# Kernel tuning notes

Hardware: AMD Instinct MI355X
Metric: run time of the kernel (lower is better)

The kernel has to match this reference:

```python
import jax, jax.numpy as jnp
import numpy as np

B, N, H, V = 8192, 12, 512, 256  # batch, n_columns, hidden_size, per-column vocab
LN_EPS = 1e-5


def setup_inputs() -> dict:
    key = jax.random.key(0)
    k0, k1, k2, k3 = jax.random.split(key, 4)
    return {
        "input_embedding": jax.random.normal(k0, (B, H), dtype=jnp.float32),
        "features": jax.random.randint(k1, (B, N), 0, V),  # one categorical id per column
        "emb_tables": jax.random.normal(k2, (N, V, H), dtype=jnp.float32) * 0.02,
        "ln_gamma": jnp.ones((2 * H,), dtype=jnp.float32),
        "ln_beta": jnp.zeros((2 * H,), dtype=jnp.float32),
        "pred_W": jax.random.normal(k3, (N, 2 * H, V), dtype=jnp.float32) * 0.02,
        "pred_b": jnp.zeros((N, V), dtype=jnp.float32),
    }


def reference(input_embedding, features, emb_tables, ln_gamma, ln_beta, pred_W, pred_b):
    n = features.shape[1]
    # per-column embedding lookup: emb[b, n] = emb_tables[n, features[b, n]]  -> [B, N, H]
    emb = emb_tables[jnp.arange(n)[None, :], features]
    # _make_masked_sums: triu(diagonal=1) mask summed over dim 1 == exclusive prefix sum
    # over the column axis: masked_sums[b, j] = sum_{i < j} emb[b, i]
    masked_sums = jnp.cumsum(emb, axis=1) - emb  # [B, N, H]
    ctx = jnp.broadcast_to(input_embedding[:, None, :], emb.shape)  # [B, N, H]
    x = jnp.concatenate([ctx, masked_sums], axis=-1)  # [B, N, 2H]
    # LayerNorm over last dim, then exact (erf) GELU as in torch nn.GELU default
    mu = jnp.mean(x, axis=-1, keepdims=True)
    var = jnp.mean(jnp.square(x - mu), axis=-1, keepdims=True)
    xn = (x - mu) * jax.lax.rsqrt(var + LN_EPS) * ln_gamma + ln_beta
    act = jax.nn.gelu(xn, approximate=False)
    # per-column predictor heads: logits[b, n, :] = act[b, n, :] @ pred_W[n] + pred_b[n]
    logits = jnp.einsum('bnh,nhv->bnv', act, pred_W) + pred_b
    return logits
```

## Files before the change

### kernel.cpp

```cpp
#include <hip/hip_runtime.h>
#include <stdint.h>

#define B_SZ 8192
#define N_F 12
#define H_DIM 512
#define K_DIM 1024
#define V_DIM 256

typedef __attribute__((ext_vector_type(8))) __bf16 bf16x8;
typedef __attribute__((ext_vector_type(4))) float f32x4;

__device__ inline float gelu_f(float x) {
  float t = 1.5957691216057308f * x * (1.0f + 0.044715f * x * x);
  return x / (1.0f + __expf(-t));
}

__device__ inline void gld_lds16(const void* g, void* l) {
  __builtin_amdgcn_global_load_lds(
      (const __attribute__((address_space(1))) void*)g,
      (__attribute__((address_space(3))) void*)l, 16, 0, 0);
}

__global__ __launch_bounds__(256, 8) void k_prep(
    const float* __restrict__ ie, const int* __restrict__ feat,
    const float* __restrict__ tab, const float* __restrict__ gam,
    const float* __restrict__ bet, __bf16* __restrict__ act2,
    float* __restrict__ stats) {
  const int lane = threadIdx.x & 63;
  const int b = blockIdx.x * 4 + (threadIdx.x >> 6);

  const float* cb = ie + (size_t)b * H_DIM + lane * 8;
  float4 c0 = *(const float4*)cb;
  float4 c1 = *(const float4*)(cb + 4);
  float s = c0.x + c0.y + c0.z + c0.w + c1.x + c1.y + c1.z + c1.w;
  float q = c0.x * c0.x + c0.y * c0.y + c0.z * c0.z + c0.w * c0.w +
            c1.x * c1.x + c1.y * c1.y + c1.z * c1.z + c1.w * c1.w;
#pragma unroll
  for (int o = 1; o < 64; o <<= 1) {
    s += __shfl_xor(s, o, 64);
    q += __shfl_xor(q, o, 64);
  }
  const float S1 = s, Q1 = q;

  const float4 g0 = *(const float4*)(gam + H_DIM + lane * 8);
  const float4 g1 = *(const float4*)(gam + H_DIM + lane * 8 + 4);
  const float4 e0 = *(const float4*)(bet + H_DIM + lane * 8);
  const float4 e1 = *(const float4*)(bet + H_DIM + lane * 8 + 4);

  float r[8];
#pragma unroll
  for (int i = 0; i < 8; ++i) r[i] = 0.f;

  const int sw = (lane & ~7) | ((lane & 7) ^ (b & 7));
  __bf16* arow = act2 + (size_t)b * H_DIM + sw * 8;

  for (int n = 0; n < N_F; ++n) {
    s = 0.f; q = 0.f;
#pragma unroll
    for (int i = 0; i < 8; ++i) { s += r[i]; q += r[i] * r[i]; }
#pragma unroll
    for (int o = 1; o < 64; o <<= 1) {
      s += __shfl_xor(s, o, 64);
      q += __shfl_xor(q, o, 64);
    }
    const float mean = (S1 + s) * (1.0f / 1024.0f);
    const float var = (Q1 + q) * (1.0f / 1024.0f) - mean * mean;
    const float rs = rsqrtf(var + 1e-5f);
    if (lane == 0)
      *(float2*)(stats + ((size_t)b * N_F + n) * 2) = make_float2(mean, rs);

    float4 t0, t1;
    const bool have = (n < N_F - 1);
    if (have) {
      const int f = feat[b * N_F + n];
      const float* tr = tab + ((size_t)n * V_DIM + f) * H_DIM + lane * 8;
      t0 = *(const float4*)tr;
      t1 = *(const float4*)(tr + 4);
    }

    bf16x8 pk;
    pk[0] = (__bf16)gelu_f((r[0] - mean) * rs * g0.x + e0.x);
    pk[1] = (__bf16)gelu_f((r[1] - mean) * rs * g0.y + e0.y);
    pk[2] = (__bf16)gelu_f((r[2] - mean) * rs * g0.z + e0.z);
    pk[3] = (__bf16)gelu_f((r[3] - mean) * rs * g0.w + e0.w);
    pk[4] = (__bf16)gelu_f((r[4] - mean) * rs * g1.x + e1.x);
    pk[5] = (__bf16)gelu_f((r[5] - mean) * rs * g1.y + e1.y);
    pk[6] = (__bf16)gelu_f((r[6] - mean) * rs * g1.z + e1.z);
    pk[7] = (__bf16)gelu_f((r[7] - mean) * rs * g1.w + e1.w);
    *(bf16x8*)(arow + (size_t)n * B_SZ * H_DIM) = pk;

    if (have) {
      r[0] += t0.x; r[1] += t0.y; r[2] += t0.z; r[3] += t0.w;
      r[4] += t1.x; r[5] += t1.y; r[6] += t1.z; r[7] += t1.w;
    }
  }
}

__global__ __launch_bounds__(256) void k_wt(const float* __restrict__ W,
                                            __bf16* __restrict__ Wt) {
  __shared__ float tile[32][33];
  const int bid = blockIdx.x;
  const int n = bid >> 8;
  const int rem = bid & 255;
  const int kt = rem >> 3, vt = rem & 7;
  const int tx = threadIdx.x & 31, ty = threadIdx.x >> 5;
  const float* src = W + (size_t)n * K_DIM * V_DIM;
#pragma unroll
  for (int i = 0; i < 4; ++i) {
    const int k = kt * 32 + ty + i * 8;
    tile[ty + i * 8][tx] = src[(size_t)k * V_DIM + vt * 32 + tx];
  }
  __syncthreads();
  __bf16* dst = Wt + (size_t)n * V_DIM * K_DIM;
  const int t = threadIdx.x;
  if (t < 128) {
    const int v_l = t >> 2, c_l = t & 3;
    const int v = vt * 32 + v_l;
    bf16x8 pk;
#pragma unroll
    for (int e = 0; e < 8; ++e) pk[e] = (__bf16)tile[c_l * 8 + e][v_l];
    const int gc = kt * 4 + c_l;
    const int swc = (gc & ~7) | ((gc & 7) ^ (v & 7));
    *(bf16x8*)(dst + (size_t)v * K_DIM + swc * 8) = pk;
  }
}

__global__ __launch_bounds__(512, 2) void k_gemm(
    const float* __restrict__ ie, const __bf16* __restrict__ act2,
    const __bf16* __restrict__ Wt, const float* __restrict__ stats,
    const float* __restrict__ gam, const float* __restrict__ bet,
    const float* __restrict__ bias, float* __restrict__ out) {
  constexpr int BM = 128, BN = 256, BK = 64;
  __shared__ __align__(16) __bf16 As[2][BM * BK];
  __shared__ __align__(16) __bf16 Ws[2][BN * BK];

  const int n = blockIdx.y;
  const int b0 = blockIdx.x * BM;
  const int t = threadIdx.x;
  const int lane = t & 63;
  const int w = t >> 6;
  const int wm = w & 1;
  const int wn = w >> 1;
  const int l15 = lane & 15;
  const int lq = lane >> 4;
  const int lr8 = lane >> 3;
  const int lo8 = lane & 7;

  const __bf16* act2n = act2 + (size_t)n * B_SZ * H_DIM;
  const __bf16* Wtn = Wt + (size_t)n * V_DIM * K_DIM;

  {
    const int k0 = 0;
#pragma unroll
    for (int p = 0; p < 4; ++p) {
      const int v0 = w * 32 + p * 8;
      gld_lds16(Wtn + (size_t)(v0 + lr8) * K_DIM + k0 + lo8 * 8,
                &Ws[0][v0 * BK]);
    }
  }

  const int pr = t >> 2;
  const int pm = t & 3;
  bf16x8 ctx[16];
  {
    const float2 st = *(const float2*)(stats + ((size_t)(b0 + pr) * N_F + n) * 2);
    const float mu = st.x, rs = st.y;
    const float* ierow = ie + (size_t)(b0 + pr) * H_DIM;
#pragma unroll
    for (int k8 = 0; k8 < 8; ++k8) {
#pragma unroll
      for (int h = 0; h < 2; ++h) {
        const int col = k8 * 64 + pm * 16 + h * 8;
        const float4 x0 = *(const float4*)(ierow + col);
        const float4 x1 = *(const float4*)(ierow + col + 4);
        const float4 gg0 = *(const float4*)(gam + col);
        const float4 gg1 = *(const float4*)(gam + col + 4);
        const float4 bb0 = *(const float4*)(bet + col);
        const float4 bb1 = *(const float4*)(bet + col + 4);
        bf16x8 pk;
        pk[0] = (__bf16)gelu_f((x0.x - mu) * rs * gg0.x + bb0.x);
        pk[1] = (__bf16)gelu_f((x0.y - mu) * rs * gg0.y + bb0.y);
        pk[2] = (__bf16)gelu_f((x0.z - mu) * rs * gg0.z + bb0.z);
        pk[3] = (__bf16)gelu_f((x0.w - mu) * rs * gg0.w + bb0.w);
        pk[4] = (__bf16)gelu_f((x1.x - mu) * rs * gg1.x + bb1.x);
        pk[5] = (__bf16)gelu_f((x1.y - mu) * rs * gg1.y + bb1.y);
        pk[6] = (__bf16)gelu_f((x1.z - mu) * rs * gg1.z + bb1.z);
        pk[7] = (__bf16)gelu_f((x1.w - mu) * rs * gg1.w + bb1.w);
        ctx[k8 * 2 + h] = pk;
      }
    }
  }

  const int sA0 = pr * BK + (((pm * 2) ^ (pr & 7)) << 3);
  const int sA1 = pr * BK + (((pm * 2 + 1) ^ (pr & 7)) << 3);

  f32x4 acc[4][4];
#pragma unroll
  for (int i = 0; i < 4; ++i)
#pragma unroll
    for (int j = 0; j < 4; ++j) acc[i][j] = (f32x4){0.f, 0.f, 0.f, 0.f};

  *(bf16x8*)(&As[0][sA0]) = ctx[0];
  *(bf16x8*)(&As[0][sA1]) = ctx[1];
  __syncthreads();

  int cur = 0;
#pragma unroll
  for (int kt = 0; kt < 16; ++kt) {
    if (kt < 15) {
      const int k0 = (kt + 1) * BK;
#pragma unroll
      for (int p = 0; p < 4; ++p) {
        const int v0 = w * 32 + p * 8;
        gld_lds16(Wtn + (size_t)(v0 + lr8) * K_DIM + k0 + lo8 * 8,
                  &Ws[cur ^ 1][v0 * BK]);
      }
      if (kt + 1 < 8) {
        *(bf16x8*)(&As[cur ^ 1][sA0]) = ctx[(kt + 1) * 2];
        *(bf16x8*)(&As[cur ^ 1][sA1]) = ctx[(kt + 1) * 2 + 1];
      } else {
#pragma unroll
        for (int p = 0; p < 2; ++p) {
          const int r0 = w * 16 + p * 8;
          gld_lds16(act2n + (size_t)(b0 + r0 + lr8) * H_DIM + (k0 - H_DIM) + lo8 * 8,
                    &As[cur ^ 1][r0 * BK]);
        }
      }
    }
#pragma unroll
    for (int ks = 0; ks < 2; ++ks) {
      const int cs = ks * 4 + lq;
      bf16x8 af[4], bb[4];
#pragma unroll
      for (int i = 0; i < 4; ++i) {
        const int row = wm * 64 + i * 16 + l15;
        af[i] = *(const bf16x8*)(&As[cur][row * BK + ((cs ^ (row & 7)) << 3)]);
      }
#pragma unroll
      for (int j = 0; j < 4; ++j) {
        const int row = wn * 64 + j * 16 + l15;
        bb[j] = *(const bf16x8*)(&Ws[cur][row * BK + ((cs ^ (row & 7)) << 3)]);
      }
#pragma unroll
      for (int i = 0; i < 4; ++i)
#pragma unroll
        for (int j = 0; j < 4; ++j)
          acc[i][j] = __builtin_amdgcn_mfma_f32_16x16x32_bf16(af[i], bb[j],
                                                              acc[i][j], 0, 0, 0);
    }
    __syncthreads();
    cur ^= 1;
  }

#pragma unroll
  for (int j = 0; j < 4; ++j) {
    const int v = wn * 64 + j * 16 + l15;
    const float bv = bias[n * V_DIM + v];
#pragma unroll
    for (int i = 0; i < 4; ++i) {
      const int rb = wm * 64 + i * 16 + lq * 4;
#pragma unroll
      for (int r = 0; r < 4; ++r) {
        out[((size_t)(b0 + rb + r) * N_F + n) * V_DIM + v] = acc[i][j][r] + bv;
      }
    }
  }
}

extern "C" void kernel_launch(void* const* d_in, const int* in_sizes, int n_in,
                              void* d_out, int out_size, void* d_ws, size_t ws_size,
                              hipStream_t stream) {
  const float* ie = (const float*)d_in[0];
  const int* feat = (const int*)d_in[1];
  const float* tab = (const float*)d_in[2];
  const float* gam = (const float*)d_in[3];
  const float* bet = (const float*)d_in[4];
  const float* predW = (const float*)d_in[5];
  const float* predb = (const float*)d_in[6];
  float* out = (float*)d_out;

  char* ws = (char*)d_ws;
  __bf16* act2 = (__bf16*)ws;
  float* stats = (float*)(ws + 100663296);
  __bf16* Wt = (__bf16*)(ws + 100663296 + 786432);

  hipLaunchKernelGGL(k_prep, dim3(B_SZ / 4), dim3(256), 0, stream, ie, feat,
                     tab, gam, bet, act2, stats);
  hipLaunchKernelGGL(k_wt, dim3(3072), dim3(256), 0, stream, predW, Wt);
  hipLaunchKernelGGL(k_gemm, dim3(B_SZ / 128, N_F), dim3(512), 0, stream, ie,
                     act2, Wt, stats, gam, bet, predb, out);
}
```

Before: 275.4 us.

## Store activations in the output buffer in place and single-buffer GEMM LDS

The bf16 activation scratch is moved into the output buffer and laid out as [b][n][h], so each (b,n) slot has the same byte size as its logits row. Each GEMM block reads only the activation rows it later overwrites with logits, which lets the workspace shrink and keeps activation and output traffic on the same addresses. To make the in-place overwrite safe and simplify the loop, the GEMM drops LDS double buffering in favour of single buffers with two barriers per K step. The risk is losing overlap between global-to-LDS loads and MFMA compute.

```diff
diff --git a/kernel.cpp b/kernel.cpp
--- a/kernel.cpp
+++ b/kernel.cpp
@@ -24,7 +24,7 @@
 __global__ __launch_bounds__(256, 8) void k_prep(
     const float* __restrict__ ie, const int* __restrict__ feat,
     const float* __restrict__ tab, const float* __restrict__ gam,
-    const float* __restrict__ bet, __bf16* __restrict__ act2,
+    const float* __restrict__ bet, __bf16* actA,
     float* __restrict__ stats) {
   const int lane = threadIdx.x & 63;
   const int b = blockIdx.x * 4 + (threadIdx.x >> 6);
@@ -52,7 +52,7 @@
   for (int i = 0; i < 8; ++i) r[i] = 0.f;
 
   const int sw = (lane & ~7) | ((lane & 7) ^ (b & 7));
-  __bf16* arow = act2 + (size_t)b * H_DIM + sw * 8;
+  __bf16* arow = actA + (size_t)b * N_F * H_DIM + sw * 8;
 
   for (int n = 0; n < N_F; ++n) {
     s = 0.f; q = 0.f;
@@ -87,7 +87,7 @@
     pk[5] = (__bf16)gelu_f((r[5] - mean) * rs * g1.y + e1.y);
     pk[6] = (__bf16)gelu_f((r[6] - mean) * rs * g1.z + e1.z);
     pk[7] = (__bf16)gelu_f((r[7] - mean) * rs * g1.w + e1.w);
-    *(bf16x8*)(arow + (size_t)n * B_SZ * H_DIM) = pk;
+    *(bf16x8*)(arow + (size_t)n * H_DIM) = pk;
 
     if (have) {
       r[0] += t0.x; r[1] += t0.y; r[2] += t0.z; r[3] += t0.w;
@@ -126,13 +126,13 @@
 }
 
 __global__ __launch_bounds__(512, 2) void k_gemm(
-    const float* __restrict__ ie, const __bf16* __restrict__ act2,
+    const float* __restrict__ ie, const __bf16* actA,
     const __bf16* __restrict__ Wt, const float* __restrict__ stats,
     const float* __restrict__ gam, const float* __restrict__ bet,
-    const float* __restrict__ bias, float* __restrict__ out) {
+    const float* __restrict__ bias, float* out) {
   constexpr int BM = 128, BN = 256, BK = 64;
-  __shared__ __align__(16) __bf16 As[2][BM * BK];
-  __shared__ __align__(16) __bf16 Ws[2][BN * BK];
+  __shared__ __align__(16) __bf16 As[BM * BK];
+  __shared__ __align__(16) __bf16 Ws[BN * BK];
 
   const int n = blockIdx.y;
   const int b0 = blockIdx.x * BM;
@@ -146,31 +146,21 @@
   const int lr8 = lane >> 3;
   const int lo8 = lane & 7;
 
-  const __bf16* act2n = act2 + (size_t)n * B_SZ * H_DIM;
   const __bf16* Wtn = Wt + (size_t)n * V_DIM * K_DIM;
 
-  {
-    const int k0 = 0;
-#pragma unroll
-    for (int p = 0; p < 4; ++p) {
-      const int v0 = w * 32 + p * 8;
-      gld_lds16(Wtn + (size_t)(v0 + lr8) * K_DIM + k0 + lo8 * 8,
-                &Ws[0][v0 * BK]);
-    }
-  }
-
-  const int pr = t >> 2;
-  const int pm = t & 3;
+  const int pr = t >> 3;
+  const int pm = t & 7;
   bf16x8 ctx[16];
   {
-    const float2 st = *(const float2*)(stats + ((size_t)(b0 + pr) * N_F + n) * 2);
-    const float mu = st.x, rs = st.y;
-    const float* ierow = ie + (size_t)(b0 + pr) * H_DIM;
-#pragma unroll
-    for (int k8 = 0; k8 < 8; ++k8) {
-#pragma unroll
-      for (int h = 0; h < 2; ++h) {
-        const int col = k8 * 64 + pm * 16 + h * 8;
+#pragma unroll
+    for (int h = 0; h < 2; ++h) {
+      const int row = b0 + pr + 64 * h;
+      const float2 st = *(const float2*)(stats + ((size_t)row * N_F + n) * 2);
+      const float mu = st.x, rs = st.y;
+      const float* ierow = ie + (size_t)row * H_DIM;
+#pragma unroll
+      for (int k8 = 0; k8 < 8; ++k8) {
+        const int col = k8 * 64 + pm * 8;
         const float4 x0 = *(const float4*)(ierow + col);
         const float4 x1 = *(const float4*)(ierow + col + 4);
         const float4 gg0 = *(const float4*)(gam + col);
@@ -191,8 +181,7 @@
     }
   }
 
-  const int sA0 = pr * BK + (((pm * 2) ^ (pr & 7)) << 3);
-  const int sA1 = pr * BK + (((pm * 2 + 1) ^ (pr & 7)) << 3);
+  const int swo = (pm ^ (pr & 7)) << 3;
 
   f32x4 acc[4][4];
 #pragma unroll
@@ -200,33 +189,28 @@
 #pragma unroll
     for (int j = 0; j < 4; ++j) acc[i][j] = (f32x4){0.f, 0.f, 0.f, 0.f};
 
-  *(bf16x8*)(&As[0][sA0]) = ctx[0];
-  *(bf16x8*)(&As[0][sA1]) = ctx[1];
-  __syncthreads();
-
-  int cur = 0;
 #pragma unroll
   for (int kt = 0; kt < 16; ++kt) {
-    if (kt < 15) {
-      const int k0 = (kt + 1) * BK;
-#pragma unroll
-      for (int p = 0; p < 4; ++p) {
-        const int v0 = w * 32 + p * 8;
-        gld_lds16(Wtn + (size_t)(v0 + lr8) * K_DIM + k0 + lo8 * 8,
-                  &Ws[cur ^ 1][v0 * BK]);
-      }
-      if (kt + 1 < 8) {
-        *(bf16x8*)(&As[cur ^ 1][sA0]) = ctx[(kt + 1) * 2];
-        *(bf16x8*)(&As[cur ^ 1][sA1]) = ctx[(kt + 1) * 2 + 1];
-      } else {
-#pragma unroll
-        for (int p = 0; p < 2; ++p) {
-          const int r0 = w * 16 + p * 8;
-          gld_lds16(act2n + (size_t)(b0 + r0 + lr8) * H_DIM + (k0 - H_DIM) + lo8 * 8,
-                    &As[cur ^ 1][r0 * BK]);
-        }
-      }
-    }
+    const int k0 = kt * BK;
+    __syncthreads();
+#pragma unroll
+    for (int p = 0; p < 4; ++p) {
+      const int v0 = w * 32 + p * 8;
+      gld_lds16(Wtn + (size_t)(v0 + lr8) * K_DIM + k0 + lo8 * 8, Ws + v0 * BK);
+    }
+    if (kt < 8) {
+      *(bf16x8*)(As + (pr)*BK + swo) = ctx[kt * 2 + 0];
+      *(bf16x8*)(As + (pr + 64) * BK + swo) = ctx[kt * 2 + 1];
+    } else {
+#pragma unroll
+      for (int p = 0; p < 2; ++p) {
+        const int r0 = w * 16 + p * 8;
+        gld_lds16(actA + ((size_t)(b0 + r0 + lr8) * N_F + n) * H_DIM +
+                      (k0 - H_DIM) + lo8 * 8,
+                  As + r0 * BK);
+      }
+    }
+    __syncthreads();
 #pragma unroll
     for (int ks = 0; ks < 2; ++ks) {
       const int cs = ks * 4 + lq;
@@ -234,12 +218,12 @@
 #pragma unroll
       for (int i = 0; i < 4; ++i) {
         const int row = wm * 64 + i * 16 + l15;
-        af[i] = *(const bf16x8*)(&As[cur][row * BK + ((cs ^ (row & 7)) << 3)]);
+        af[i] = *(const bf16x8*)(As + row * BK + ((cs ^ (row & 7)) << 3));
       }
 #pragma unroll
       for (int j = 0; j < 4; ++j) {
         const int row = wn * 64 + j * 16 + l15;
-        bb[j] = *(const bf16x8*)(&Ws[cur][row * BK + ((cs ^ (row & 7)) << 3)]);
+        bb[j] = *(const bf16x8*)(Ws + row * BK + ((cs ^ (row & 7)) << 3));
       }
 #pragma unroll
       for (int i = 0; i < 4; ++i)
@@ -248,8 +232,6 @@
           acc[i][j] = __builtin_amdgcn_mfma_f32_16x16x32_bf16(af[i], bb[j],
                                                               acc[i][j], 0, 0, 0);
     }
-    __syncthreads();
-    cur ^= 1;
   }
 
 #pragma unroll
@@ -279,14 +261,15 @@
   const float* predb = (const float*)d_in[6];
   float* out = (float*)d_out;
 
+  __bf16* actA = (__bf16*)d_out;
+
   char* ws = (char*)d_ws;
-  __bf16* act2 = (__bf16*)ws;
-  float* stats = (float*)(ws + 100663296);
-  __bf16* Wt = (__bf16*)(ws + 100663296 + 786432);
+  float* stats = (float*)ws;
+  __bf16* Wt = (__bf16*)(ws + 786432);
 
   hipLaunchKernelGGL(k_prep, dim3(B_SZ / 4), dim3(256), 0, stream, ie, feat,
-                     tab, gam, bet, act2, stats);
+                     tab, gam, bet, actA, stats);
   hipLaunchKernelGGL(k_wt, dim3(3072), dim3(256), 0, stream, predW, Wt);
   hipLaunchKernelGGL(k_gemm, dim3(B_SZ / 128, N_F), dim3(512), 0, stream, ie,
-                     act2, Wt, stats, gam, bet, predb, out);
-}
+                     actA, Wt, stats, gam, bet, predb, out);
+}
```

New measurement: 273.0 us. Within noise of the previous version (-0.9%).
